# Optimization experiments

Hardware: AMD Instinct MI355X
Metric: run time of the kernel (lower is better)

## Reference

```python
import jax, jax.numpy as jnp
import numpy as np

B, N, D = 16, 1024, 768
H = 12
HD = D // H           # 64
NUM_BUCKETS = 49      # iRPE 'product' buckets, shared across heads
SCALE = HD ** -0.5


def setup_inputs() -> dict:
    key = jax.random.key(0)
    k1, k2, k3, k4, k5, k6 = jax.random.split(key, 6)
    x = jax.random.normal(k1, (B, N, D), dtype=jnp.float32)
    qkv_w = jax.random.normal(k2, (3 * D, D), dtype=jnp.float32) * 0.02
    rpe_table = jax.random.normal(k3, (NUM_BUCKETS, HD), dtype=jnp.float32) * 0.02
    rp_bucket = jax.random.randint(k4, (N, N), 0, NUM_BUCKETS, dtype=jnp.int32)
    proj_w = jax.random.normal(k5, (D, D), dtype=jnp.float32) * 0.02
    proj_b = jax.random.normal(k6, (D,), dtype=jnp.float32) * 0.02
    return {"x": x, "qkv_w": qkv_w, "rpe_table": rpe_table,
            "rp_bucket": rp_bucket, "proj_w": proj_w, "proj_b": proj_b}


def reference(x, qkv_w, rpe_table, rp_bucket, proj_w, proj_b):
    b, n, d = x.shape
    # qkv projection (no bias), split into q,k,v of shape [B,H,N,HD]
    qkv = (x @ qkv_w.T).reshape(b, n, 3, H, HD)
    qkv = jnp.transpose(qkv, (2, 0, 3, 1, 4))
    q, k, v = qkv[0], qkv[1], qkv[2]
    q = q * SCALE
    # full attention scores [B,H,N,N]
    attn = jnp.einsum('bhid,bhjd->bhij', q, k)
    # iRPE contextual bias on keys: project q onto the bucket table, then
    # gather per relative-position bucket: bias[b,h,i,j] = (q @ W^T)[b,h,i,rp_bucket[i,j]]
    bias_all = jnp.einsum('bhid,cd->bhic', q, rpe_table)   # [B,H,N,num_buckets]
    bias = bias_all[:, :, jnp.arange(n)[:, None], rp_bucket]  # [B,H,N,N]
    attn = jax.nn.softmax(attn + bias, axis=-1)
    out = jnp.einsum('bhij,bhjd->bhid', attn, v)            # [B,H,N,HD]
    out = jnp.transpose(out, (0, 2, 1, 3)).reshape(b, n, d)
    return out @ proj_w.T + proj_b
```

## Files before the change

### kernel.cpp

```cpp
#include <hip/hip_runtime.h>

typedef short bf16x8 __attribute__((ext_vector_type(8)));
typedef float f32x4 __attribute__((ext_vector_type(4)));

#define QSCALE 0.1803368801111204f

__device__ __forceinline__ unsigned short f2bf(float f){
  unsigned u = __float_as_uint(f);
  u = (u + 0x7fffu + ((u >> 16) & 1u)) >> 16;
  return (unsigned short)u;
}
__device__ __forceinline__ f32x4 mfma16(bf16x8 a, bf16x8 b, f32x4 c){
  return __builtin_amdgcn_mfma_f32_16x16x32_bf16(a, b, c, 0, 0, 0);
}
__device__ __forceinline__ void gload_lds16(const void* g, void* l){
  __builtin_amdgcn_global_load_lds((__attribute__((address_space(1))) void*)(g),
                                   (__attribute__((address_space(3))) void*)(l), 16, 0, 0);
}
__device__ __forceinline__ unsigned cvt_pk_bf16(float lo, float hi){
  unsigned r;
  asm("v_cvt_pk_bf16_f32 %0, %1, %2" : "=v"(r) : "v"(lo), "v"(hi));
  return r;
}
__device__ __forceinline__ float exp2_fast(float x){
  float r;
  asm("v_exp_f32 %0, %1" : "=v"(r) : "v"(x));
  return r;
}

__global__ __launch_bounds__(256) void prep_kernel(
    const float* __restrict__ x, const float* __restrict__ qw,
    const float* __restrict__ pw, const int* __restrict__ rp,
    unsigned short* __restrict__ xb, unsigned short* __restrict__ wb,
    unsigned short* __restrict__ pwb, unsigned char* __restrict__ rp8){
  const int T1 = 3145728;
  const int T2 = T1 + 442368;
  const int T3 = T2 + 147456;
  const int T4 = T3 + 262144;
  for (int t = blockIdx.x * 256 + threadIdx.x; t < T4; t += gridDim.x * 256){
    if (t < T3){
      const float4* src; ushort4* dst; int off;
      if (t < T1){ src = (const float4*)x;  dst = (ushort4*)xb;  off = t; }
      else if (t < T2){ src = (const float4*)qw; dst = (ushort4*)wb;  off = t - T1; }
      else { src = (const float4*)pw; dst = (ushort4*)pwb; off = t - T2; }
      float4 v = src[off];
      ushort4 u;
      u.x = f2bf(v.x); u.y = f2bf(v.y); u.z = f2bf(v.z); u.w = f2bf(v.w);
      dst[off] = u;
    } else {
      int off = t - T3;
      int4 v = ((const int4*)rp)[off];
      int row = (off * 4) >> 10;
      int sw = (row & 7) << 4;
      uchar4 u;
      u.x = (unsigned char)((v.x << 1) ^ sw);
      u.y = (unsigned char)((v.y << 1) ^ sw);
      u.z = (unsigned char)((v.z << 1) ^ sw);
      u.w = (unsigned char)((v.w << 1) ^ sw);
      ((uchar4*)rp8)[off] = u;
    }
  }
}

__device__ __forceinline__ void gemm_core(
    const unsigned short* __restrict__ A, const unsigned short* __restrict__ Bm,
    int m0, int n0, int K, unsigned short* As, unsigned short* Bs,
    f32x4 (&acc)[4][4]){
  const int tid = threadIdx.x, lane = tid & 63, wave = tid >> 6;
  const int g = lane >> 4, r16 = lane & 15;
  const int wr = wave >> 1, wc = wave & 1;
  for (int k0 = 0; k0 < K; k0 += 32){
    __syncthreads();
    #pragma unroll
    for (int j = 0; j < 2; j++){
      int ci = j * 256 + tid;
      int row = ci >> 2, c = ci & 3;
      gload_lds16(A  + (size_t)(m0 + row) * K + k0 + c * 8,
                  (char*)As + (j * 256 + wave * 64) * 16);
      gload_lds16(Bm + (size_t)(n0 + row) * K + k0 + c * 8,
                  (char*)Bs + (j * 256 + wave * 64) * 16);
    }
    __syncthreads();
    bf16x8 a[4], b[4];
    #pragma unroll
    for (int mi = 0; mi < 4; mi++)
      a[mi] = *(const bf16x8*)((const char*)As + (wr * 64 + mi * 16 + r16) * 64 + g * 16);
    #pragma unroll
    for (int ni = 0; ni < 4; ni++)
      b[ni] = *(const bf16x8*)((const char*)Bs + (wc * 64 + ni * 16 + r16) * 64 + g * 16);
    #pragma unroll
    for (int mi = 0; mi < 4; mi++)
      #pragma unroll
      for (int ni = 0; ni < 4; ni++)
        acc[mi][ni] = mfma16(a[mi], b[ni], acc[mi][ni]);
  }
}

__global__ __launch_bounds__(256) void qkv_gemm(
    const unsigned short* __restrict__ xb, const unsigned short* __restrict__ wb,
    unsigned short* __restrict__ q_s, unsigned short* __restrict__ k_s,
    unsigned short* __restrict__ v_t){
  __shared__ __align__(16) unsigned short As[128 * 32];
  __shared__ __align__(16) unsigned short Bs[128 * 32];
  f32x4 acc[4][4];
  #pragma unroll
  for (int i = 0; i < 4; i++)
    #pragma unroll
    for (int j = 0; j < 4; j++){
      acc[i][j][0] = 0.f; acc[i][j][1] = 0.f; acc[i][j][2] = 0.f; acc[i][j][3] = 0.f;
    }
  const int m0 = blockIdx.y * 128, n0 = blockIdx.x * 128;
  gemm_core(xb, wb, m0, n0, 768, As, Bs, acc);

  const int lane = threadIdx.x & 63, wave = threadIdx.x >> 6;
  const int g = lane >> 4, r16 = lane & 15;
  const int wr = wave >> 1, wc = wave & 1;
  #pragma unroll
  for (int mi = 0; mi < 4; mi++){
    #pragma unroll
    for (int ni = 0; ni < 4; ni++){
      int gcol = n0 + wc * 64 + ni * 16 + r16;
      int sel = gcol / 768;
      int rem = gcol - sel * 768;
      int h = rem >> 6, hd = rem & 63;
      #pragma unroll
      for (int r = 0; r < 4; r++){
        int grow = m0 + wr * 64 + mi * 16 + 4 * g + r;
        int bb = grow >> 10, ii = grow & 1023;
        size_t base = ((size_t)(bb * 12 + h)) << 16;
        float v = acc[mi][ni][r];
        if (sel == 0)      q_s[base + ((size_t)ii << 6) + hd] = f2bf(v * QSCALE);
        else if (sel == 1) k_s[base + ((size_t)ii << 6) + hd] = f2bf(v);
        else               v_t[base + ((size_t)hd << 10) + ii] = f2bf(v);
      }
    }
  }
}

__global__ __launch_bounds__(256) void attn_kernel(
    const unsigned short* __restrict__ q_s, const unsigned short* __restrict__ k_s,
    const unsigned short* __restrict__ v_t, const unsigned char* __restrict__ rp8,
    const float* __restrict__ rpe, unsigned short* __restrict__ ao){
  __shared__ __align__(16) char smem[49152];
  const int tid = threadIdx.x, lane = tid & 63, w = tid >> 6;
  const int g = lane >> 4, r16 = lane & 15;
  const int qb = blockIdx.x, bh = blockIdx.y;
  const size_t bh_base = (size_t)bh << 16;
  const int iw = w * 32;

  const size_t q0 = bh_base + ((size_t)(qb * 128 + iw + r16) << 6);
  bf16x8 qf[4];
  qf[0] = *(const bf16x8*)(q_s + q0 + g * 8);
  qf[1] = *(const bf16x8*)(q_s + q0 + 32 + g * 8);
  qf[2] = *(const bf16x8*)(q_s + q0 + 1024 + g * 8);
  qf[3] = *(const bf16x8*)(q_s + q0 + 1024 + 32 + g * 8);

  char* bias_lds = smem + 32768;
  #pragma unroll
  for (int jt = 0; jt < 4; jt++){
    int crow = jt * 16 + r16;
    bf16x8 a0, a1;
    #pragma unroll
    for (int e = 0; e < 8; e++){ a0[e] = 0; a1[e] = 0; }
    if (crow < 49){
      const float* rr = rpe + crow * 64 + g * 8;
      float4 x0 = *(const float4*)(rr);
      float4 x1 = *(const float4*)(rr + 4);
      float4 y0 = *(const float4*)(rr + 32);
      float4 y1 = *(const float4*)(rr + 36);
      a0[0]=f2bf(x0.x); a0[1]=f2bf(x0.y); a0[2]=f2bf(x0.z); a0[3]=f2bf(x0.w);
      a0[4]=f2bf(x1.x); a0[5]=f2bf(x1.y); a0[6]=f2bf(x1.z); a0[7]=f2bf(x1.w);
      a1[0]=f2bf(y0.x); a1[1]=f2bf(y0.y); a1[2]=f2bf(y0.z); a1[3]=f2bf(y0.w);
      a1[4]=f2bf(y1.x); a1[5]=f2bf(y1.y); a1[6]=f2bf(y1.z); a1[7]=f2bf(y1.w);
    }
    #pragma unroll
    for (int h = 0; h < 2; h++){
      f32x4 z = {0.f, 0.f, 0.f, 0.f};
      z = mfma16(a0, qf[2 * h], z);
      z = mfma16(a1, qf[2 * h + 1], z);
      int irow = iw + h * 16 + r16;
      uint2 u; u.x = cvt_pk_bf16(z[0], z[1]); u.y = cvt_pk_bf16(z[2], z[3]);
      *(uint2*)(bias_lds + irow * 128 + ((jt * 32 + 8 * g) ^ ((r16 & 7) << 4))) = u;
    }
  }
  const char* brow0 = bias_lds + (iw + r16) * 128;
  const char* brow1 = brow0 + 16 * 128;

  unsigned short* ks = (unsigned short*)smem;
  unsigned short* vs = (unsigned short*)(smem + 8192);
  char* pbuf = smem + 16384 + w * 4096;

  const int ci0 = tid, ci1 = 256 + tid;
  const int row0 = ci0 >> 3, sc0 = (ci0 & 7) ^ (row0 & 7);
  const int row1 = ci1 >> 3, sc1 = (ci1 & 7) ^ (row1 & 7);
  const char* kp0 = (const char*)(k_s + bh_base) + row0 * 128 + sc0 * 16;
  const char* kp1 = (const char*)(k_s + bh_base) + row1 * 128 + sc1 * 16;
  const char* vp0 = (const char*)(v_t + bh_base) + row0 * 2048 + sc0 * 16;
  const char* vp1 = (const char*)(v_t + bh_base) + row1 * 2048 + sc1 * 16;
  char* kl0 = (char*)smem + w * 1024;
  char* kl1 = (char*)smem + 4096 + w * 1024;
  char* vl0 = (char*)smem + 8192 + w * 1024;
  char* vl1 = (char*)smem + 12288 + w * 1024;
  const unsigned char* rprow0 = rp8 + ((size_t)(qb * 128 + iw + r16) << 10);
  const unsigned char* rprow1 = rprow0 + (16 << 10);

  f32x4 o[8];
  #pragma unroll
  for (int t = 0; t < 8; t++){ o[t][0]=0.f; o[t][1]=0.f; o[t][2]=0.f; o[t][3]=0.f; }
  float m0 = -INFINITY, m1 = -INFINITY, l0 = 0.f, l1 = 0.f;

  for (int kb = 0; kb < 16; kb++){
    __syncthreads();
    gload_lds16(kp0, kl0);
    gload_lds16(kp1, kl1);
    gload_lds16(vp0, vl0);
    gload_lds16(vp1, vl1);
    kp0 += 8192; kp1 += 8192; vp0 += 128; vp1 += 128;
    __syncthreads();

    f32x4 st0[4], st1[4];
    #pragma unroll
    for (int jt = 0; jt < 4; jt++){
      int krow = jt * 16 + r16;
      int sw = (krow & 7) << 4;
      bf16x8 ka0 = *(const bf16x8*)((char*)ks + krow * 128 + ((g * 16) ^ sw));
      bf16x8 ka1 = *(const bf16x8*)((char*)ks + krow * 128 + ((64 + g * 16) ^ sw));
      f32x4 z0 = {0.f, 0.f, 0.f, 0.f};
      z0 = mfma16(ka0, qf[0], z0);
      z0 = mfma16(ka1, qf[1], z0);
      st0[jt] = z0;
      f32x4 z1 = {0.f, 0.f, 0.f, 0.f};
      z1 = mfma16(ka0, qf[2], z1);
      z1 = mfma16(ka1, qf[3], z1);
      st1[jt] = z1;
    }
    #pragma unroll
    for (int jt = 0; jt < 4; jt++){
      unsigned bu0 = *(const unsigned*)(rprow0 + kb * 64 + jt * 16 + g * 4);
      unsigned bu1 = *(const unsigned*)(rprow1 + kb * 64 + jt * 16 + g * 4);
      st0[jt][0] += __uint_as_float((unsigned)*(const unsigned short*)(brow0 + (bu0 & 0xff)) << 16);
      st0[jt][1] += __uint_as_float((unsigned)*(const unsigned short*)(brow0 + ((bu0 >> 8) & 0xff)) << 16);
      st0[jt][2] += __uint_as_float((unsigned)*(const unsigned short*)(brow0 + ((bu0 >> 16) & 0xff)) << 16);
      st0[jt][3] += __uint_as_float((unsigned)*(const unsigned short*)(brow0 + (bu0 >> 24)) << 16);
      st1[jt][0] += __uint_as_float((unsigned)*(const unsigned short*)(brow1 + (bu1 & 0xff)) << 16);
      st1[jt][1] += __uint_as_float((unsigned)*(const unsigned short*)(brow1 + ((bu1 >> 8) & 0xff)) << 16);
      st1[jt][2] += __uint_as_float((unsigned)*(const unsigned short*)(brow1 + ((bu1 >> 16) & 0xff)) << 16);
      st1[jt][3] += __uint_as_float((unsigned)*(const unsigned short*)(brow1 + (bu1 >> 24)) << 16);
    }
    float t0 = -INFINITY, t1 = -INFINITY;
    #pragma unroll
    for (int jt = 0; jt < 4; jt++){
      t0 = fmaxf(t0, fmaxf(fmaxf(st0[jt][0], st0[jt][1]), fmaxf(st0[jt][2], st0[jt][3])));
      t1 = fmaxf(t1, fmaxf(fmaxf(st1[jt][0], st1[jt][1]), fmaxf(st1[jt][2], st1[jt][3])));
    }
    t0 = fmaxf(t0, __shfl_xor(t0, 16)); t0 = fmaxf(t0, __shfl_xor(t0, 32));
    t1 = fmaxf(t1, __shfl_xor(t1, 16)); t1 = fmaxf(t1, __shfl_xor(t1, 32));
    const bool skip = __all(t0 <= m0 + 8.f && t1 <= m1 + 8.f);
    if (!skip){
      float m0n = fmaxf(m0, t0), m1n = fmaxf(m1, t1);
      float a0 = exp2_fast(m0 - m0n), a1 = exp2_fast(m1 - m1n);
      m0 = m0n; m1 = m1n;
      l0 *= a0; l1 *= a1;
      float af0[4], af1[4];
      #pragma unroll
      for (int r = 0; r < 4; r++){ af0[r] = __shfl(a0, 4 * g + r); af1[r] = __shfl(a1, 4 * g + r); }
      #pragma unroll
      for (int dt = 0; dt < 4; dt++){
        o[dt][0] *= af0[0]; o[dt][1] *= af0[1]; o[dt][2] *= af0[2]; o[dt][3] *= af0[3];
        o[4+dt][0] *= af1[0]; o[4+dt][1] *= af1[1]; o[4+dt][2] *= af1[2]; o[4+dt][3] *= af1[3];
      }
    }
    #pragma unroll
    for (int jt = 0; jt < 4; jt++){
      float p0 = exp2_fast(st0[jt][0] - m0);
      float p1 = exp2_fast(st0[jt][1] - m0);
      float p2 = exp2_fast(st0[jt][2] - m0);
      float p3 = exp2_fast(st0[jt][3] - m0);
      l0 += (p0 + p1) + (p2 + p3);
      uint2 u; u.x = cvt_pk_bf16(p0, p1); u.y = cvt_pk_bf16(p2, p3);
      *(uint2*)(pbuf + r16 * 128 + ((jt * 32 + g * 8) ^ ((r16 & 7) << 4))) = u;
      float q0_ = exp2_fast(st1[jt][0] - m1);
      float q1_ = exp2_fast(st1[jt][1] - m1);
      float q2_ = exp2_fast(st1[jt][2] - m1);
      float q3_ = exp2_fast(st1[jt][3] - m1);
      l1 += (q0_ + q1_) + (q2_ + q3_);
      uint2 v; v.x = cvt_pk_bf16(q0_, q1_); v.y = cvt_pk_bf16(q2_, q3_);
      *(uint2*)(pbuf + (16 + r16) * 128 + ((jt * 32 + g * 8) ^ ((r16 & 7) << 4))) = v;
    }
    #pragma unroll
    for (int kt = 0; kt < 2; kt++){
      bf16x8 pa0 = *(const bf16x8*)(pbuf + r16 * 128 + ((kt * 64 + g * 16) ^ ((r16 & 7) << 4)));
      bf16x8 pa1 = *(const bf16x8*)(pbuf + (16 + r16) * 128 + ((kt * 64 + g * 16) ^ ((r16 & 7) << 4)));
      #pragma unroll
      for (int dt = 0; dt < 4; dt++){
        int vrow = dt * 16 + r16;
        bf16x8 vb = *(const bf16x8*)((char*)vs + vrow * 128 + ((kt * 64 + g * 16) ^ ((vrow & 7) << 4)));
        o[dt] = mfma16(pa0, vb, o[dt]);
        o[4+dt] = mfma16(pa1, vb, o[4+dt]);
      }
    }
  }

  l0 += __shfl_xor(l0, 16); l0 += __shfl_xor(l0, 32);
  l1 += __shfl_xor(l1, 16); l1 += __shfl_xor(l1, 32);
  float lf0[4], lf1[4];
  #pragma unroll
  for (int r = 0; r < 4; r++){
    lf0[r] = 1.f / __shfl(l0, 4 * g + r);
    lf1[r] = 1.f / __shfl(l1, 4 * g + r);
  }
  const int bidx = bh / 12, hh = bh - bidx * 12;
  #pragma unroll
  for (int h = 0; h < 2; h++){
    #pragma unroll
    for (int dt = 0; dt < 4; dt++){
      int d = dt * 16 + r16;
      #pragma unroll
      for (int r = 0; r < 4; r++){
        int i = qb * 128 + iw + h * 16 + 4 * g + r;
        float val = o[h * 4 + dt][r] * (h ? lf1[r] : lf0[r]);
        ao[(size_t)(bidx * 1024 + i) * 768 + hh * 64 + d] = f2bf(val);
      }
    }
  }
}

__global__ __launch_bounds__(256) void proj_gemm(
    const unsigned short* __restrict__ aob, const unsigned short* __restrict__ pwb,
    const float* __restrict__ pb, float* __restrict__ out){
  __shared__ __align__(16) unsigned short As[128 * 32];
  __shared__ __align__(16) unsigned short Bs[128 * 32];
  f32x4 acc[4][4];
  #pragma unroll
  for (int i = 0; i < 4; i++)
    #pragma unroll
    for (int j = 0; j < 4; j++){
      acc[i][j][0] = 0.f; acc[i][j][1] = 0.f; acc[i][j][2] = 0.f; acc[i][j][3] = 0.f;
    }
  const int m0 = blockIdx.y * 128, n0 = blockIdx.x * 128;
  gemm_core(aob, pwb, m0, n0, 768, As, Bs, acc);

  const int lane = threadIdx.x & 63, wave = threadIdx.x >> 6;
  const int g = lane >> 4, r16 = lane & 15;
  const int wr = wave >> 1, wc = wave & 1;
  #pragma unroll
  for (int mi = 0; mi < 4; mi++){
    #pragma unroll
    for (int ni = 0; ni < 4; ni++){
      int gcol = n0 + wc * 64 + ni * 16 + r16;
      float bias = pb[gcol];
      #pragma unroll
      for (int r = 0; r < 4; r++){
        int grow = m0 + wr * 64 + mi * 16 + 4 * g + r;
        out[(size_t)grow * 768 + gcol] = acc[mi][ni][r] + bias;
      }
    }
  }
}

extern "C" void kernel_launch(void* const* d_in, const int* in_sizes, int n_in,
                              void* d_out, int out_size, void* d_ws, size_t ws_size,
                              hipStream_t stream){
  const float* x      = (const float*)d_in[0];
  const float* qkv_w  = (const float*)d_in[1];
  const float* rpe    = (const float*)d_in[2];
  const int*   rp     = (const int*)d_in[3];
  const float* proj_w = (const float*)d_in[4];
  const float* proj_b = (const float*)d_in[5];
  float* out = (float*)d_out;
  char* ws = (char*)d_ws;

  unsigned short* xb  = (unsigned short*)(ws);
  unsigned short* wb  = (unsigned short*)(ws + 25165824);
  unsigned short* pwb = (unsigned short*)(ws + 28704768);
  unsigned char*  rp8 = (unsigned char*) (ws + 29884416);
  unsigned short* q_s = (unsigned short*)(ws + 30932992);
  unsigned short* k_s = (unsigned short*)(ws + 56098816);
  unsigned short* v_t = (unsigned short*)(ws + 81264640);
  unsigned short* aob = (unsigned short*)(ws + 106430464);

  prep_kernel<<<2048, 256, 0, stream>>>(x, qkv_w, proj_w, rp, xb, wb, pwb, rp8);
  qkv_gemm<<<dim3(18, 128), 256, 0, stream>>>(xb, wb, q_s, k_s, v_t);
  attn_kernel<<<dim3(8, 192), 256, 0, stream>>>(q_s, k_s, v_t, rp8, rpe, aob);
  proj_gemm<<<dim3(6, 128), 256, 0, stream>>>(aob, pwb, proj_b, out);
}
```

Measured before the change: 307.1 us.

## Load K/V fragments directly from global into registers and remap blocks per XCD

The attention kernel no longer stages K and V tiles in shared memory with global_load_lds and two barriers per iteration. Each wave now loads its MFMA fragments straight from global memory into registers, which shrinks LDS from 48 KB to 32 KB and removes the per-iteration syncs. The grid is flattened to 1D, and the block index is remapped so all query blocks of a head land on the same XCD, which should improve L2 reuse of K/V. In exchange, each of the four waves fetches the same K/V data separately, adding cache traffic and register pressure.

```diff
diff --git a/kernel.cpp b/kernel.cpp
--- a/kernel.cpp
+++ b/kernel.cpp
@@ -141,10 +141,12 @@
     const unsigned short* __restrict__ q_s, const unsigned short* __restrict__ k_s,
     const unsigned short* __restrict__ v_t, const unsigned char* __restrict__ rp8,
     const float* __restrict__ rpe, unsigned short* __restrict__ ao){
-  __shared__ __align__(16) char smem[49152];
+  __shared__ __align__(16) char smem[32768];
   const int tid = threadIdx.x, lane = tid & 63, w = tid >> 6;
   const int g = lane >> 4, r16 = lane & 15;
-  const int qb = blockIdx.x, bh = blockIdx.y;
+  const int b = blockIdx.x;
+  const int xcd = b & 7, kk = b >> 3;
+  const int bh = xcd * 24 + (kk >> 3), qb = kk & 7;
   const size_t bh_base = (size_t)bh << 16;
   const int iw = w * 32;
 
@@ -155,7 +157,7 @@
   qf[2] = *(const bf16x8*)(q_s + q0 + 1024 + g * 8);
   qf[3] = *(const bf16x8*)(q_s + q0 + 1024 + 32 + g * 8);
 
-  char* bias_lds = smem + 32768;
+  char* bias_lds = smem + 16384;
   #pragma unroll
   for (int jt = 0; jt < 4; jt++){
     int crow = jt * 16 + r16;
@@ -186,53 +188,44 @@
   const char* brow0 = bias_lds + (iw + r16) * 128;
   const char* brow1 = brow0 + 16 * 128;
 
-  unsigned short* ks = (unsigned short*)smem;
-  unsigned short* vs = (unsigned short*)(smem + 8192);
-  char* pbuf = smem + 16384 + w * 4096;
-
-  const int ci0 = tid, ci1 = 256 + tid;
-  const int row0 = ci0 >> 3, sc0 = (ci0 & 7) ^ (row0 & 7);
-  const int row1 = ci1 >> 3, sc1 = (ci1 & 7) ^ (row1 & 7);
-  const char* kp0 = (const char*)(k_s + bh_base) + row0 * 128 + sc0 * 16;
-  const char* kp1 = (const char*)(k_s + bh_base) + row1 * 128 + sc1 * 16;
-  const char* vp0 = (const char*)(v_t + bh_base) + row0 * 2048 + sc0 * 16;
-  const char* vp1 = (const char*)(v_t + bh_base) + row1 * 2048 + sc1 * 16;
-  char* kl0 = (char*)smem + w * 1024;
-  char* kl1 = (char*)smem + 4096 + w * 1024;
-  char* vl0 = (char*)smem + 8192 + w * 1024;
-  char* vl1 = (char*)smem + 12288 + w * 1024;
+  char* pbuf = smem + w * 4096;
   const unsigned char* rprow0 = rp8 + ((size_t)(qb * 128 + iw + r16) << 10);
   const unsigned char* rprow1 = rprow0 + (16 << 10);
 
+  const unsigned short* kbase = k_s + bh_base + r16 * 64 + g * 8;
+  const unsigned short* vbase = v_t + bh_base + r16 * 1024 + g * 8;
+
   f32x4 o[8];
   #pragma unroll
   for (int t = 0; t < 8; t++){ o[t][0]=0.f; o[t][1]=0.f; o[t][2]=0.f; o[t][3]=0.f; }
   float m0 = -INFINITY, m1 = -INFINITY, l0 = 0.f, l1 = 0.f;
 
   for (int kb = 0; kb < 16; kb++){
-    __syncthreads();
-    gload_lds16(kp0, kl0);
-    gload_lds16(kp1, kl1);
-    gload_lds16(vp0, vl0);
-    gload_lds16(vp1, vl1);
-    kp0 += 8192; kp1 += 8192; vp0 += 128; vp1 += 128;
-    __syncthreads();
-
+    const unsigned short* kp = kbase + kb * 4096;
+    bf16x8 ka0[4], ka1[4];
+    #pragma unroll
+    for (int jt = 0; jt < 4; jt++){
+      ka0[jt] = *(const bf16x8*)(kp + jt * 1024);
+      ka1[jt] = *(const bf16x8*)(kp + jt * 1024 + 32);
+    }
     f32x4 st0[4], st1[4];
     #pragma unroll
     for (int jt = 0; jt < 4; jt++){
-      int krow = jt * 16 + r16;
-      int sw = (krow & 7) << 4;
-      bf16x8 ka0 = *(const bf16x8*)((char*)ks + krow * 128 + ((g * 16) ^ sw));
-      bf16x8 ka1 = *(const bf16x8*)((char*)ks + krow * 128 + ((64 + g * 16) ^ sw));
       f32x4 z0 = {0.f, 0.f, 0.f, 0.f};
-      z0 = mfma16(ka0, qf[0], z0);
-      z0 = mfma16(ka1, qf[1], z0);
+      z0 = mfma16(ka0[jt], qf[0], z0);
+      z0 = mfma16(ka1[jt], qf[1], z0);
       st0[jt] = z0;
       f32x4 z1 = {0.f, 0.f, 0.f, 0.f};
-      z1 = mfma16(ka0, qf[2], z1);
-      z1 = mfma16(ka1, qf[3], z1);
+      z1 = mfma16(ka0[jt], qf[2], z1);
+      z1 = mfma16(ka1[jt], qf[3], z1);
       st1[jt] = z1;
+    }
+    const unsigned short* vp = vbase + kb * 64;
+    bf16x8 vb0[4], vb1[4];
+    #pragma unroll
+    for (int dt = 0; dt < 4; dt++){
+      vb0[dt] = *(const bf16x8*)(vp + dt * 16384);
+      vb1[dt] = *(const bf16x8*)(vp + dt * 16384 + 32);
     }
     #pragma unroll
     for (int jt = 0; jt < 4; jt++){
@@ -293,8 +286,7 @@
       bf16x8 pa1 = *(const bf16x8*)(pbuf + (16 + r16) * 128 + ((kt * 64 + g * 16) ^ ((r16 & 7) << 4)));
       #pragma unroll
       for (int dt = 0; dt < 4; dt++){
-        int vrow = dt * 16 + r16;
-        bf16x8 vb = *(const bf16x8*)((char*)vs + vrow * 128 + ((kt * 64 + g * 16) ^ ((vrow & 7) << 4)));
+        bf16x8 vb = kt ? vb1[dt] : vb0[dt];
         o[dt] = mfma16(pa0, vb, o[dt]);
         o[4+dt] = mfma16(pa1, vb, o[4+dt]);
       }
@@ -381,6 +373,6 @@
 
   prep_kernel<<<2048, 256, 0, stream>>>(x, qkv_w, proj_w, rp, xb, wb, pwb, rp8);
   qkv_gemm<<<dim3(18, 128), 256, 0, stream>>>(xb, wb, q_s, k_s, v_t);
-  attn_kernel<<<dim3(8, 192), 256, 0, stream>>>(q_s, k_s, v_t, rp8, rpe, aob);
+  attn_kernel<<<1536, 256, 0, stream>>>(q_s, k_s, v_t, rp8, rpe, aob);
   proj_gemm<<<dim3(6, 128), 256, 0, stream>>>(aob, pwb, proj_b, out);
 }
```

After: 429.0 us. +39.7%, slower.
